# Optimization experiments

Measured on AMD Instinct MI355X. Metric: run time of the kernel, lower is better.

The kernel has to match this reference:

```python
import jax, jax.numpy as jnp
import numpy as np

B, S, D = 8, 2048, 256
H = 4
DH = D // H  # 64


def setup_inputs() -> dict:
    key = jax.random.key(0)
    ks = jax.random.split(key, 6)
    x = jax.random.normal(ks[0], (B, S, D), dtype=jnp.float32)
    # Linear weights stored as (d_in, d_out) so y = x @ W (+ b)
    scale = 1.0 / np.sqrt(D)
    w_q = jax.random.normal(ks[1], (D, D), dtype=jnp.float32) * scale
    w_k = jax.random.normal(ks[2], (D, D), dtype=jnp.float32) * scale
    w_v = jax.random.normal(ks[3], (D, D), dtype=jnp.float32) * scale
    w_o = jax.random.normal(ks[4], (D, D), dtype=jnp.float32) * scale
    b_o = jax.random.normal(ks[5], (D,), dtype=jnp.float32) * 0.01
    return {"x": x, "w_q": w_q, "w_k": w_k, "w_v": w_v, "w_o": w_o, "b_o": b_o}


def reference(x, w_q, w_k, w_v, w_o, b_o):
    b, s, _ = x.shape
    # project and split heads: [b, h, s, dh]
    q = (x @ w_q).reshape(b, s, H, DH).transpose(0, 2, 1, 3)
    k = (x @ w_k).reshape(b, s, H, DH).transpose(0, 2, 1, 3)
    v = (x @ w_v).reshape(b, s, H, DH).transpose(0, 2, 1, 3)
    # full attention matrix [b, h, s, s] (matches original non-fused math)
    scores = jnp.einsum('bhqd,bhkd->bhqk', q, k) / jnp.sqrt(jnp.float32(DH))
    attn = jax.nn.softmax(scores, axis=-1)  # dropout is identity in eval
    ctx = jnp.einsum('bhqk,bhkd->bhqd', attn, v)
    ctx = ctx.transpose(0, 2, 1, 3).reshape(b, s, H * DH)
    return ctx @ w_o + b_o
```

## Files before the change

kernel.cpp:

```cpp
#include <hip/hip_runtime.h>
#include <hip/hip_fp16.h>
#include <math.h>

typedef _Float16 f16;
typedef _Float16 f16x8 __attribute__((ext_vector_type(8)));
typedef float f32x4 __attribute__((ext_vector_type(4)));

#define BB 8
#define SS 2048
#define DD 256
#define HH 4
#define DHH 64

#define LOG2E 1.44269504088896340736f
#define MOFF (4.0f * LOG2E)

__global__ __launch_bounds__(256) void prep_kernel(
    const float* __restrict__ wq, const float* __restrict__ wk,
    const float* __restrict__ wv, const float* __restrict__ wo,
    f16* __restrict__ wqkvT, f16* __restrict__ woT) {
  __shared__ f16 lds[64][72];
  int dout0 = blockIdx.x * 64;
  int k0 = blockIdx.y * 64;
  const float* src;
  f16* dst;
  int col0, drow;
  if (dout0 < 256)      { src = wq; dst = wqkvT; col0 = dout0;       drow = dout0; }
  else if (dout0 < 512) { src = wk; dst = wqkvT; col0 = dout0 - 256; drow = dout0; }
  else if (dout0 < 768) { src = wv; dst = wqkvT; col0 = dout0 - 512; drow = dout0; }
  else                  { src = wo; dst = woT;   col0 = dout0 - 768; drow = dout0 - 768; }

  int dl = threadIdx.x & 63, kl = threadIdx.x >> 6;
#pragma unroll
  for (int i = 0; i < 16; i++) {
    int kloc = i * 4 + kl;
    lds[kloc][dl] = (f16)src[(size_t)(k0 + kloc) * 256 + col0 + dl];
  }
  __syncthreads();
  int row_l = threadIdx.x >> 2, kq = threadIdx.x & 3;
  f16x8 v0, v1;
#pragma unroll
  for (int j = 0; j < 8; j++) v0[j] = lds[kq * 16 + j][row_l];
#pragma unroll
  for (int j = 0; j < 8; j++) v1[j] = lds[kq * 16 + 8 + j][row_l];
  f16* p = dst + (size_t)(drow + row_l) * 256 + k0 + kq * 16;
  *(f16x8*)p = v0;
  *(f16x8*)(p + 8) = v1;
}

__global__ __launch_bounds__(256) void qkv_gemm(
    const float* __restrict__ x, const f16* __restrict__ wT,
    f16* __restrict__ Q, f16* __restrict__ K, f16* __restrict__ VT) {
  __shared__ __attribute__((aligned(16))) f16 bstage[8][4][64][8];
  __shared__ __attribute__((aligned(16))) f16 lds_t[64][72];
  int m0 = blockIdx.x * 64;
  int which = blockIdx.y;
  int nbase = which * 256;
  int wave = threadIdx.x >> 6, lane = threadIdx.x & 63;
  int lm = lane & 15, quad = lane >> 4;

  const float* arow = x + (size_t)(m0 + wave * 16 + lm) * 256 + quad * 8;
  f16x8 a[8];
#pragma unroll
  for (int kk = 0; kk < 8; kk++) {
    f32x4 a0 = *(const f32x4*)(arow + kk * 32);
    f32x4 a1 = *(const f32x4*)(arow + kk * 32 + 4);
#pragma unroll
    for (int j = 0; j < 4; j++) { a[kk][j] = (f16)a0[j]; a[kk][j + 4] = (f16)a1[j]; }
  }

  f16x8 breg[8];
  auto bload = [&](int n0) {
#pragma unroll
    for (int kk = 0; kk < 8; kk++)
      breg[kk] = *(const f16x8*)(wT + (size_t)(n0 + wave * 16 + lm) * 256 + kk * 32 + quad * 8);
  };
  bload(nbase);

  int bb = m0 >> 11, s0 = m0 & 2047;
  for (int i = 0; i < 4; i++) {
    int n0 = nbase + i * 64;
#pragma unroll
    for (int kk = 0; kk < 8; kk++)
      *(f16x8*)&bstage[kk][wave][lane][0] = breg[kk];
    __syncthreads();
    if (i + 1 < 4) bload(nbase + (i + 1) * 64);

    f32x4 acc[4] = {};
#pragma unroll
    for (int kk = 0; kk < 8; kk++)
#pragma unroll
      for (int nt = 0; nt < 4; nt++) {
        f16x8 b = *(const f16x8*)&bstage[kk][nt][lane][0];
        acc[nt] = __builtin_amdgcn_mfma_f32_16x16x32_f16(a[kk], b, acc[nt], 0, 0, 0);
      }

    if (which < 2) {
      f16* dst = (which == 0) ? Q : K;
      int nb = n0 & 255;
#pragma unroll
      for (int nt = 0; nt < 4; nt++) {
        int dout = nb + nt * 16 + lm;
        int h = dout >> 6, dh = dout & 63;
#pragma unroll
        for (int r = 0; r < 4; r++) {
          int s = s0 + wave * 16 + quad * 4 + r;
          dst[(((size_t)(bb * HH + h) * SS + s) << 6) + dh] = (f16)acc[nt][r];
        }
      }
    } else {
      int h = i;
#pragma unroll
      for (int nt = 0; nt < 4; nt++)
#pragma unroll
        for (int r = 0; r < 4; r++)
          lds_t[nt * 16 + lm][wave * 16 + quad * 4 + r] = (f16)acc[nt][r];
      __syncthreads();
      int rr = threadIdx.x >> 2, cc = threadIdx.x & 3;
      f16* vrow = VT + ((size_t)(bb * HH + h) * DHH + rr) * SS + s0;
      f16x8 v0 = *(const f16x8*)&lds_t[rr][cc * 16];
      f16x8 v1 = *(const f16x8*)&lds_t[rr][cc * 16 + 8];
      *(f16x8*)(vrow + cc * 16) = v0;
      *(f16x8*)(vrow + cc * 16 + 8) = v1;
    }
    __syncthreads();
  }
}

__global__ __launch_bounds__(512) void attn_kernel(
    const f16* __restrict__ Q, const f16* __restrict__ K,
    const f16* __restrict__ VT, f16* __restrict__ ctx) {
  __shared__ __attribute__((aligned(16))) f16 kbuf[2][8][64][8];
  __shared__ __attribute__((aligned(16))) f16 vbuf[2][8][64][8];
  __shared__ __attribute__((aligned(16))) f16 lds_p[8][16][72];

  int qb = blockIdx.x, h = blockIdx.y, b = blockIdx.z;
  int wave = threadIdx.x >> 6, lane = threadIdx.x & 63;
  int lm = lane & 15, quad = lane >> 4;
  const f16* Qbh = Q + (size_t)(b * HH + h) * SS * DHH;
  const f16* Kbh = K + (size_t)(b * HH + h) * SS * DHH;
  const f16* Vbh = VT + (size_t)(b * HH + h) * DHH * SS;
  int q0 = qb * 128 + wave * 16;

  int kpf = wave >> 2, ntf = wave & 3;
  f16x8 tk, tv;
  auto stage_load = [&](int key0) {
    tk = *(const f16x8*)(Kbh + (key0 + ntf * 16 + lm) * DHH + kpf * 32 + quad * 8);
    tv = *(const f16x8*)(Vbh + (ntf * 16 + lm) * SS + key0 + kpf * 32 + quad * 8);
  };
  auto stage_write = [&](int buf) {
    *(f16x8*)&kbuf[buf][wave][lane][0] = tk;
    *(f16x8*)&vbuf[buf][wave][lane][0] = tv;
  };

  f16x8 aq[2];
#pragma unroll
  for (int kp = 0; kp < 2; kp++) {
    aq[kp] = *(const f16x8*)(Qbh + (q0 + lm) * DHH + kp * 32 + quad * 8);
#pragma unroll
    for (int j = 0; j < 8; j++) aq[kp][j] *= (f16)0.125f;
  }
  f16x8 vones;
#pragma unroll
  for (int j = 0; j < 8; j++) vones[j] = (f16)1.0f;

  f32x4 accO[4] = {};
  f32x4 accL = {};

  stage_load(0);
  stage_write(0);
  stage_load(64);

  const int NT = SS / 64;
  for (int t = 0; t < NT; t++) {
    int cur = t & 1;
    __syncthreads();

    if (t + 1 < NT) {
      stage_write(cur ^ 1);
      if (t + 2 < NT) stage_load((t + 2) * 64);
    }

    f32x4 accS[4] = {};
#pragma unroll
    for (int kp = 0; kp < 2; kp++)
#pragma unroll
      for (int nt = 0; nt < 4; nt++) {
        f16x8 bk = *(const f16x8*)&kbuf[cur][kp * 4 + nt][lane][0];
        accS[nt] = __builtin_amdgcn_mfma_f32_16x16x32_f16(aq[kp], bk, accS[nt], 0, 0, 0);
      }

#pragma unroll
    for (int nt = 0; nt < 4; nt++)
#pragma unroll
      for (int r = 0; r < 4; r++) {
        float p = __builtin_amdgcn_exp2f(__builtin_fmaf(accS[nt][r], LOG2E, -MOFF));
        lds_p[wave][quad * 4 + r][nt * 16 + lm] = (f16)p;
      }

#pragma unroll
    for (int kp = 0; kp < 2; kp++) {
      f16x8 ap = *(const f16x8*)&lds_p[wave][lm][kp * 32 + quad * 8];
      accL = __builtin_amdgcn_mfma_f32_16x16x32_f16(ap, vones, accL, 0, 0, 0);
#pragma unroll
      for (int nt = 0; nt < 4; nt++) {
        f16x8 bv = *(const f16x8*)&vbuf[cur][kp * 4 + nt][lane][0];
        accO[nt] = __builtin_amdgcn_mfma_f32_16x16x32_f16(ap, bv, accO[nt], 0, 0, 0);
      }
    }
  }

  float rinv[4];
#pragma unroll
  for (int r = 0; r < 4; r++) rinv[r] = 1.0f / accL[r];
#pragma unroll
  for (int nt = 0; nt < 4; nt++)
#pragma unroll
    for (int r = 0; r < 4; r++) {
      int s = q0 + quad * 4 + r;
      ctx[(size_t)(b * SS + s) * DD + h * DHH + nt * 16 + lm] =
          (f16)(accO[nt][r] * rinv[r]);
    }
}

__global__ __launch_bounds__(256) void out_gemm(
    const f16* __restrict__ ctxh, const f16* __restrict__ woT,
    const float* __restrict__ bo, float* __restrict__ out) {
  __shared__ __attribute__((aligned(16))) f16 bstage[8][4][64][8];
  int m0 = blockIdx.x * 64;
  int nbase = blockIdx.y * 128;
  int wave = threadIdx.x >> 6, lane = threadIdx.x & 63;
  int lm = lane & 15, quad = lane >> 4;
  const f16* arow = ctxh + (size_t)(m0 + wave * 16 + lm) * 256 + quad * 8;
  f16x8 a[8];
#pragma unroll
  for (int kk = 0; kk < 8; kk++) a[kk] = *(const f16x8*)(arow + kk * 32);

  f16x8 breg[8];
  auto bload = [&](int n0) {
#pragma unroll
    for (int kk = 0; kk < 8; kk++)
      breg[kk] = *(const f16x8*)(woT + (size_t)(n0 + wave * 16 + lm) * 256 + kk * 32 + quad * 8);
  };
  bload(nbase);

  for (int i = 0; i < 2; i++) {
    int n0 = nbase + i * 64;
#pragma unroll
    for (int kk = 0; kk < 8; kk++)
      *(f16x8*)&bstage[kk][wave][lane][0] = breg[kk];
    __syncthreads();
    if (i + 1 < 2) bload(nbase + 64);

    f32x4 acc[4] = {};
#pragma unroll
    for (int kk = 0; kk < 8; kk++)
#pragma unroll
      for (int nt = 0; nt < 4; nt++) {
        f16x8 bfr = *(const f16x8*)&bstage[kk][nt][lane][0];
        acc[nt] = __builtin_amdgcn_mfma_f32_16x16x32_f16(a[kk], bfr, acc[nt], 0, 0, 0);
      }
#pragma unroll
    for (int nt = 0; nt < 4; nt++) {
      int dout = n0 + nt * 16 + lm;
      float bias = bo[dout];
#pragma unroll
      for (int r = 0; r < 4; r++) {
        int t = m0 + wave * 16 + quad * 4 + r;
        out[(size_t)t * 256 + dout] = acc[nt][r] + bias;
      }
    }
    __syncthreads();
  }
}

extern "C" void kernel_launch(void* const* d_in, const int* in_sizes, int n_in,
                              void* d_out, int out_size, void* d_ws, size_t ws_size,
                              hipStream_t stream) {
  const float* x  = (const float*)d_in[0];
  const float* wq = (const float*)d_in[1];
  const float* wk = (const float*)d_in[2];
  const float* wv = (const float*)d_in[3];
  const float* wo = (const float*)d_in[4];
  const float* bo = (const float*)d_in[5];
  float* out = (float*)d_out;

  char* ws = (char*)d_ws;
  const size_t SZ = 8388608;
  f16* Qb    = (f16*)(ws);
  f16* Kb    = (f16*)(ws + SZ);
  f16* VTb   = (f16*)(ws + 2 * SZ);
  f16* ctxh  = (f16*)(ws + 3 * SZ);
  f16* wqkvT = (f16*)(ws + 4 * SZ);
  f16* woT   = (f16*)(ws + 4 * SZ + 393216);

  hipLaunchKernelGGL(prep_kernel, dim3(16, 4), dim3(256), 0, stream,
                     wq, wk, wv, wo, wqkvT, woT);
  hipLaunchKernelGGL(qkv_gemm, dim3(256, 3), dim3(256), 0, stream,
                     x, wqkvT, Qb, Kb, VTb);
  hipLaunchKernelGGL(attn_kernel, dim3(16, 4, 8), dim3(512), 0, stream,
                     Qb, Kb, VTb, ctxh);
  hipLaunchKernelGGL(out_gemm, dim3(256, 2), dim3(256), 0, stream,
                     ctxh, woT, bo, out);
}
```

Before: 158.7 us.

## Rewrite attention core with 32x32 MFMA, register-resident P via permlane swap

Attention now uses 4 waves of 32 queries each with 32x32x16 MFMA instructions, computing S transposed so the exponentiated probabilities can be repacked into A-operand layout with permlane32_swap instead of a round trip through LDS. The softmax scale and log2e are folded into Q in the QKV GEMM, and the fixed max offset is loaded as the MFMA accumulator init, which removes a per-element FMA. The fp16 conversion uses packed round-toward-zero and the final division uses a fast reciprocal. This removes the LDS traffic for P and some VALU work, at the cost of larger accumulators, register pressure and different occupancy.

```diff
diff --git a/kernel.cpp b/kernel.cpp
--- a/kernel.cpp
+++ b/kernel.cpp
@@ -5,6 +5,9 @@
 typedef _Float16 f16;
 typedef _Float16 f16x8 __attribute__((ext_vector_type(8)));
 typedef float f32x4 __attribute__((ext_vector_type(4)));
+typedef float f32x16 __attribute__((ext_vector_type(16)));
+typedef unsigned int u32;
+typedef unsigned int u32x4 __attribute__((ext_vector_type(4)));
 
 #define BB 8
 #define SS 2048
@@ -13,7 +16,13 @@
 #define DHH 64
 
 #define LOG2E 1.44269504088896340736f
-#define MOFF (4.0f * LOG2E)
+#define MOFF2 (4.0f * LOG2E)
+#define QSCALE (0.125f * LOG2E)
+
+static __device__ __forceinline__ u32 pkrtz(float a, float b) {
+  auto t = __builtin_amdgcn_cvt_pkrtz(a, b);
+  return __builtin_bit_cast(u32, t);
+}
 
 __global__ __launch_bounds__(256) void prep_kernel(
     const float* __restrict__ wq, const float* __restrict__ wk,
@@ -58,6 +67,7 @@
   int nbase = which * 256;
   int wave = threadIdx.x >> 6, lane = threadIdx.x & 63;
   int lm = lane & 15, quad = lane >> 4;
+  float qsc = (which == 0) ? QSCALE : 1.0f;
 
   const float* arow = x + (size_t)(m0 + wave * 16 + lm) * 256 + quad * 8;
   f16x8 a[8];
@@ -105,7 +115,7 @@
 #pragma unroll
         for (int r = 0; r < 4; r++) {
           int s = s0 + wave * 16 + quad * 4 + r;
-          dst[(((size_t)(bb * HH + h) * SS + s) << 6) + dh] = (f16)acc[nt][r];
+          dst[(((size_t)(bb * HH + h) * SS + s) << 6) + dh] = (f16)(acc[nt][r] * qsc);
         }
       }
     } else {
@@ -127,45 +137,50 @@
   }
 }
 
-__global__ __launch_bounds__(512) void attn_kernel(
+__global__ __launch_bounds__(256, 2) void attn_kernel(
     const f16* __restrict__ Q, const f16* __restrict__ K,
     const f16* __restrict__ VT, f16* __restrict__ ctx) {
   __shared__ __attribute__((aligned(16))) f16 kbuf[2][8][64][8];
   __shared__ __attribute__((aligned(16))) f16 vbuf[2][8][64][8];
-  __shared__ __attribute__((aligned(16))) f16 lds_p[8][16][72];
-
-  int qb = blockIdx.x, h = blockIdx.y, b = blockIdx.z;
-  int wave = threadIdx.x >> 6, lane = threadIdx.x & 63;
-  int lm = lane & 15, quad = lane >> 4;
-  const f16* Qbh = Q + (size_t)(b * HH + h) * SS * DHH;
-  const f16* Kbh = K + (size_t)(b * HH + h) * SS * DHH;
-  const f16* Vbh = VT + (size_t)(b * HH + h) * DHH * SS;
-  int q0 = qb * 128 + wave * 16;
-
-  int kpf = wave >> 2, ntf = wave & 3;
-  f16x8 tk, tv;
+
+  int qb = blockIdx.x, hd = blockIdx.y, b = blockIdx.z;
+  int w = threadIdx.x >> 6, lane = threadIdx.x & 63;
+  int l31 = lane & 31, hi = lane >> 5, hi8 = hi * 8;
+  const f16* Qbh = Q + (size_t)(b * HH + hd) * SS * DHH;
+  const f16* Kbh = K + (size_t)(b * HH + hd) * SS * DHH;
+  const f16* Vbh = VT + (size_t)(b * HH + hd) * DHH * SS;
+  int q0 = qb * 128 + w * 32;
+
+  f16x8 tk0, tk1, tv0, tv1;
   auto stage_load = [&](int key0) {
-    tk = *(const f16x8*)(Kbh + (key0 + ntf * 16 + lm) * DHH + kpf * 32 + quad * 8);
-    tv = *(const f16x8*)(Vbh + (ntf * 16 + lm) * SS + key0 + kpf * 32 + quad * 8);
+    tk0 = *(const f16x8*)(Kbh + (size_t)(key0 + l31) * DHH + w * 16 + hi8);
+    tk1 = *(const f16x8*)(Kbh + (size_t)(key0 + 32 + l31) * DHH + w * 16 + hi8);
+    tv0 = *(const f16x8*)(Vbh + (size_t)l31 * SS + key0 + w * 16 + hi8);
+    tv1 = *(const f16x8*)(Vbh + (size_t)(32 + l31) * SS + key0 + w * 16 + hi8);
   };
   auto stage_write = [&](int buf) {
-    *(f16x8*)&kbuf[buf][wave][lane][0] = tk;
-    *(f16x8*)&vbuf[buf][wave][lane][0] = tv;
+    *(f16x8*)&kbuf[buf][w][lane][0] = tk0;
+    *(f16x8*)&kbuf[buf][4 + w][lane][0] = tk1;
+    *(f16x8*)&vbuf[buf][w][lane][0] = tv0;
+    *(f16x8*)&vbuf[buf][4 + w][lane][0] = tv1;
   };
 
-  f16x8 aq[2];
-#pragma unroll
-  for (int kp = 0; kp < 2; kp++) {
-    aq[kp] = *(const f16x8*)(Qbh + (q0 + lm) * DHH + kp * 32 + quad * 8);
-#pragma unroll
-    for (int j = 0; j < 8; j++) aq[kp][j] *= (f16)0.125f;
+  f16x8 aq[4];
+  {
+    const f16* qrow = Qbh + (size_t)(q0 + l31) * DHH + hi8;
+#pragma unroll
+    for (int kp = 0; kp < 4; kp++) aq[kp] = *(const f16x8*)(qrow + kp * 16);
   }
   f16x8 vones;
 #pragma unroll
   for (int j = 0; j < 8; j++) vones[j] = (f16)1.0f;
-
-  f32x4 accO[4] = {};
-  f32x4 accL = {};
+  f32x16 minit;
+#pragma unroll
+  for (int r = 0; r < 16; r++) minit[r] = -MOFF2;
+
+  f32x16 accO0, accO1, accL;
+#pragma unroll
+  for (int r = 0; r < 16; r++) { accO0[r] = 0.f; accO1[r] = 0.f; accL[r] = 0.f; }
 
   stage_load(0);
   stage_write(0);
@@ -181,46 +196,58 @@
       if (t + 2 < NT) stage_load((t + 2) * 64);
     }
 
-    f32x4 accS[4] = {};
-#pragma unroll
-    for (int kp = 0; kp < 2; kp++)
-#pragma unroll
-      for (int nt = 0; nt < 4; nt++) {
-        f16x8 bk = *(const f16x8*)&kbuf[cur][kp * 4 + nt][lane][0];
-        accS[nt] = __builtin_amdgcn_mfma_f32_16x16x32_f16(aq[kp], bk, accS[nt], 0, 0, 0);
-      }
-
-#pragma unroll
-    for (int nt = 0; nt < 4; nt++)
-#pragma unroll
-      for (int r = 0; r < 4; r++) {
-        float p = __builtin_amdgcn_exp2f(__builtin_fmaf(accS[nt][r], LOG2E, -MOFF));
-        lds_p[wave][quad * 4 + r][nt * 16 + lm] = (f16)p;
-      }
-
-#pragma unroll
-    for (int kp = 0; kp < 2; kp++) {
-      f16x8 ap = *(const f16x8*)&lds_p[wave][lm][kp * 32 + quad * 8];
-      accL = __builtin_amdgcn_mfma_f32_16x16x32_f16(ap, vones, accL, 0, 0, 0);
-#pragma unroll
-      for (int nt = 0; nt < 4; nt++) {
-        f16x8 bv = *(const f16x8*)&vbuf[cur][kp * 4 + nt][lane][0];
-        accO[nt] = __builtin_amdgcn_mfma_f32_16x16x32_f16(ap, bv, accO[nt], 0, 0, 0);
-      }
-    }
-  }
-
-  float rinv[4];
-#pragma unroll
-  for (int r = 0; r < 4; r++) rinv[r] = 1.0f / accL[r];
-#pragma unroll
-  for (int nt = 0; nt < 4; nt++)
-#pragma unroll
-    for (int r = 0; r < 4; r++) {
-      int s = q0 + quad * 4 + r;
-      ctx[(size_t)(b * SS + s) * DD + h * DHH + nt * 16 + lm] =
-          (f16)(accO[nt][r] * rinv[r]);
-    }
+    f32x16 accST[2];
+#pragma unroll
+    for (int kp = 0; kp < 4; kp++)
+#pragma unroll
+      for (int nt = 0; nt < 2; nt++) {
+        f16x8 kf = *(const f16x8*)&kbuf[cur][nt * 4 + kp][lane][0];
+        accST[nt] = __builtin_amdgcn_mfma_f32_32x32x16_f16(
+            kf, aq[kp], kp == 0 ? minit : accST[nt], 0, 0, 0);
+      }
+
+    f16x8 pa[4];
+#pragma unroll
+    for (int nt = 0; nt < 2; nt++) {
+      u32 u[4][2];
+#pragma unroll
+      for (int bq = 0; bq < 4; bq++) {
+        float p0 = __builtin_amdgcn_exp2f(accST[nt][4 * bq + 0]);
+        float p1 = __builtin_amdgcn_exp2f(accST[nt][4 * bq + 1]);
+        float p2 = __builtin_amdgcn_exp2f(accST[nt][4 * bq + 2]);
+        float p3 = __builtin_amdgcn_exp2f(accST[nt][4 * bq + 3]);
+        u[bq][0] = pkrtz(p0, p1);
+        u[bq][1] = pkrtz(p2, p3);
+      }
+#pragma unroll
+      for (int sl = 0; sl < 2; sl++) {
+        auto r0 = __builtin_amdgcn_permlane32_swap(u[2 * sl][0], u[2 * sl + 1][0],
+                                                   false, false);
+        auto r1 = __builtin_amdgcn_permlane32_swap(u[2 * sl][1], u[2 * sl + 1][1],
+                                                   false, false);
+        u32x4 wv = {(u32)r0[0], (u32)r1[0], (u32)r0[1], (u32)r1[1]};
+        pa[nt * 2 + sl] = __builtin_bit_cast(f16x8, wv);
+      }
+    }
+
+#pragma unroll
+    for (int ks = 0; ks < 4; ks++) {
+      accL = __builtin_amdgcn_mfma_f32_32x32x16_f16(pa[ks], vones, accL, 0, 0, 0);
+      f16x8 v0 = *(const f16x8*)&vbuf[cur][ks][lane][0];
+      accO0 = __builtin_amdgcn_mfma_f32_32x32x16_f16(pa[ks], v0, accO0, 0, 0, 0);
+      f16x8 v1 = *(const f16x8*)&vbuf[cur][4 + ks][lane][0];
+      accO1 = __builtin_amdgcn_mfma_f32_32x32x16_f16(pa[ks], v1, accO1, 0, 0, 0);
+    }
+  }
+
+#pragma unroll
+  for (int r = 0; r < 16; r++) {
+    float rinv = __builtin_amdgcn_rcpf(accL[r]);
+    int s = q0 + (r & 3) + 8 * (r >> 2) + 4 * hi;
+    f16* dst = ctx + (size_t)(b * SS + s) * DD + hd * DHH + l31;
+    dst[0]  = (f16)(accO0[r] * rinv);
+    dst[32] = (f16)(accO1[r] * rinv);
+  }
 }
 
 __global__ __launch_bounds__(256) void out_gemm(
@@ -298,7 +325,7 @@
                      wq, wk, wv, wo, wqkvT, woT);
   hipLaunchKernelGGL(qkv_gemm, dim3(256, 3), dim3(256), 0, stream,
                      x, wqkvT, Qb, Kb, VTb);
-  hipLaunchKernelGGL(attn_kernel, dim3(16, 4, 8), dim3(512), 0, stream,
+  hipLaunchKernelGGL(attn_kernel, dim3(16, 4, 8), dim3(256), 0, stream,
                      Qb, Kb, VTb, ctxh);
   hipLaunchKernelGGL(out_gemm, dim3(256, 2), dim3(256), 0, stream,
                      ctxh, woT, bo, out);
```

New measurement: 151.8 us. 4.4% less time.
